# Kernel tuning notes

Hardware: AMD Instinct MI355X
Metric: run time of the kernel (lower is better)

Reference implementation:

```python
import jax, jax.numpy as jnp
import numpy as np

T, B, D, H = 1024, 128, 256, 256


def setup_inputs() -> dict:
    key = jax.random.key(0)
    ks = jax.random.split(key, 16)
    s_in = 1.0 / np.sqrt(D + H)  # torch Linear default init scale
    inp = {
        "inputs": jax.random.normal(ks[0], (T, B, D), dtype=jnp.float32),
        "Wf": jax.random.uniform(ks[1], (H, D + H), jnp.float32, -s_in, s_in),
        "bf": jax.random.uniform(ks[2], (H,), jnp.float32, -s_in, s_in),
        "Wi": jax.random.uniform(ks[3], (H, D + H), jnp.float32, -s_in, s_in),
        "bi": jax.random.uniform(ks[4], (H,), jnp.float32, -s_in, s_in),
        "Wg": jax.random.uniform(ks[5], (H, D + H), jnp.float32, -s_in, s_in),
        "bg": jax.random.uniform(ks[6], (H,), jnp.float32, -s_in, s_in),
        "Wo": jax.random.uniform(ks[7], (H, D + H), jnp.float32, -s_in, s_in),
        "bo": jax.random.uniform(ks[8], (H,), jnp.float32, -s_in, s_in),
        # estimator params stacked over the 4 gates (order: f, i, g, o)
        "estW1": jax.random.uniform(ks[9], (4, 8, H), jnp.float32, -1/np.sqrt(H), 1/np.sqrt(H)),
        "estb1": jax.random.uniform(ks[10], (4, 8), jnp.float32, -1/np.sqrt(H), 1/np.sqrt(H)),
        "estW2": jax.random.uniform(ks[11], (4, 4, 8), jnp.float32, -1/np.sqrt(8), 1/np.sqrt(8)),
        "estb2": jax.random.uniform(ks[12], (4, 4), jnp.float32, -1/np.sqrt(8), 1/np.sqrt(8)),
        "estW3": jax.random.uniform(ks[13], (4, 1, 4), jnp.float32, -0.5, 0.5),
        "estb3": jax.random.uniform(ks[14], (4, 1), jnp.float32, -0.5, 0.5),
    }
    return inp


def reference(inputs, Wf, bf, Wi, bi, Wg, bg, Wo, bo,
              estW1, estb1, estW2, estb2, estW3, estb3):
    def est(x, k):
        # tiny MLP: H -> 8 -> 4 -> 1 with tanh/tanh/sigmoid
        h1 = jnp.tanh(x @ estW1[k].T + estb1[k])
        h2 = jnp.tanh(h1 @ estW2[k].T + estb2[k])
        return jax.nn.sigmoid(h2 @ estW3[k].T + estb3[k])  # [B, 1]

    def step(carry, x):
        hx, cx = carry
        comb = jnp.concatenate([x, hx], axis=1)  # [B, D+H]
        f = jax.nn.sigmoid(comb @ Wf.T + bf)
        i = jax.nn.sigmoid(comb @ Wi.T + bi)
        g = jnp.tanh(comb @ Wg.T + bg)
        o = jax.nn.sigmoid(comb @ Wo.T + bo)
        f = f * est(f, 0)
        i = i * est(i, 1)
        g = g * est(g, 2)
        o = o * est(o, 3)
        cx = f * cx + i * g
        hx = o * jnp.tanh(cx)
        return (hx, cx), hx

    hx0 = jnp.zeros((B, H), dtype=inputs.dtype)
    cx0 = jnp.zeros((B, H), dtype=inputs.dtype)
    (hx, cx), stacked = jax.lax.scan(step, (hx0, cx0), inputs)
    return stacked, hx, cx
```

## Files before the change

### kernel.cpp

```cpp
#include <hip/hip_runtime.h>
#include <hip/hip_fp16.h>
#include <math.h>

#define T_STEPS 1024
#define BATCH   128
#define D_IN    256
#define H_DIM   256
#define NCOL    1024

typedef _Float16 half2_t __attribute__((ext_vector_type(2)));

__device__ __forceinline__ float sigmoidf_(float x) {
    return 1.0f / (1.0f + __expf(-x));
}

__device__ __forceinline__ float tanhf_(float x) {
    float ax = fabsf(x);
    float t = __expf(-2.0f * ax);
    float r = (1.0f - t) / (1.0f + t);
    return copysignf(r, x);
}

__device__ __forceinline__ float dot2f(unsigned int w, unsigned int h, float acc) {
#if __has_builtin(__builtin_amdgcn_fdot2)
    return __builtin_amdgcn_fdot2(__builtin_bit_cast(half2_t, w),
                                  __builtin_bit_cast(half2_t, h), acc, false);
#else
    __half2 wv = *(__half2*)&w, hv = *(__half2*)&h;
    acc = fmaf(__half2float(wv.x), __half2float(hv.x), acc);
    return fmaf(__half2float(wv.y), __half2float(hv.y), acc);
#endif
}

__device__ __forceinline__ unsigned int packh2(float a, float b) {
    __half2 p = __floats2half2_rn(a, b);
    return *(unsigned int*)&p;
}

__global__ __launch_bounds__(256) void prep_kernel(
    const float* __restrict__ Wf, const float* __restrict__ Wi,
    const float* __restrict__ Wg, const float* __restrict__ Wo,
    const float* __restrict__ bf, const float* __restrict__ bi,
    const float* __restrict__ bg, const float* __restrict__ bo,
    unsigned int* __restrict__ WX2, uint4* __restrict__ WX4,
    uint4* __restrict__ WH4, float* __restrict__ biasc)
{
    int idx = blockIdx.x * 256 + threadIdx.x;
    int m = idx >> 10;
    int j = idx & 1023;
    int g = j >> 8;
    int h = j & 255;
    const float* W = (g == 0) ? Wf : (g == 1) ? Wi : (g == 2) ? Wg : Wo;
    const float* row = W + h * (D_IN + H_DIM);
    const float* rx = row + 8 * m;
    const float* rh = row + D_IN + 8 * m;
    uint4 vx = make_uint4(packh2(rx[0], rx[1]), packh2(rx[2], rx[3]),
                          packh2(rx[4], rx[5]), packh2(rx[6], rx[7]));
    uint4 vh = make_uint4(packh2(rh[0], rh[1]), packh2(rh[2], rh[3]),
                          packh2(rh[4], rh[5]), packh2(rh[6], rh[7]));
    WX4[idx] = vx;
    WH4[idx] = vh;
    unsigned int* d = (unsigned int*)&vx;
    #pragma unroll
    for (int p = 0; p < 4; p++) WX2[(4 * m + p) * 1024 + j] = d[p];
    if (idx < NCOL) {
        const float* bb = (g == 0) ? bf : (g == 1) ? bi : (g == 2) ? bg : bo;
        biasc[j] = bb[h];
    }
}

__global__ __launch_bounds__(256) void pregemm_kernel(
    const float* __restrict__ x, const unsigned int* __restrict__ WX2,
    const float* __restrict__ biasc, float* __restrict__ pre) {
    __shared__ float xs[16 * 256];
    const int tid = threadIdx.x;
    const size_t r0 = (size_t)blockIdx.x * 16;

    {
        const float4* xsrc = (const float4*)(x + r0 * D_IN);
        float4* xd = (float4*)xs;
        #pragma unroll
        for (int i = 0; i < 4; i++) xd[tid + 256 * i] = xsrc[tid + 256 * i];
    }
    float4 b4 = ((const float4*)biasc)[tid];
    float a[16][4];
    #pragma unroll
    for (int r = 0; r < 16; r++) {
        a[r][0] = b4.x; a[r][1] = b4.y; a[r][2] = b4.z; a[r][3] = b4.w;
    }
    __syncthreads();

    const uint4* wp = (const uint4*)WX2;
    const float2* xs2 = (const float2*)xs;
    #pragma unroll 2
    for (int k2 = 0; k2 < 128; k2++) {
        uint4 wv = wp[k2 * 256 + tid];
        __half2 q0 = *(__half2*)&wv.x, q1 = *(__half2*)&wv.y;
        __half2 q2 = *(__half2*)&wv.z, q3 = *(__half2*)&wv.w;
        float w0l = __half2float(q0.x), w0h = __half2float(q0.y);
        float w1l = __half2float(q1.x), w1h = __half2float(q1.y);
        float w2l = __half2float(q2.x), w2h = __half2float(q2.y);
        float w3l = __half2float(q3.x), w3h = __half2float(q3.y);
        #pragma unroll
        for (int r = 0; r < 16; r++) {
            float2 xv = xs2[r * 128 + k2];
            a[r][0] = fmaf(xv.x, w0l, a[r][0]); a[r][0] = fmaf(xv.y, w0h, a[r][0]);
            a[r][1] = fmaf(xv.x, w1l, a[r][1]); a[r][1] = fmaf(xv.y, w1h, a[r][1]);
            a[r][2] = fmaf(xv.x, w2l, a[r][2]); a[r][2] = fmaf(xv.y, w2h, a[r][2]);
            a[r][3] = fmaf(xv.x, w3l, a[r][3]); a[r][3] = fmaf(xv.y, w3h, a[r][3]);
        }
    }
    #pragma unroll
    for (int r = 0; r < 16; r++) {
        ((float4*)(pre + (r0 + r) * NCOL))[tid] =
            make_float4(a[r][0], a[r][1], a[r][2], a[r][3]);
    }
}

__global__ __launch_bounds__(1024) void qlstm_kernel(
    const float* __restrict__ x,
    const uint4* __restrict__ WX4,
    const uint4* __restrict__ WH4,
    const float* __restrict__ biasc,
    const float* __restrict__ pre, int use_pre,
    const float* __restrict__ estW1, const float* __restrict__ estb1,
    const float* __restrict__ estW2, const float* __restrict__ estb2,
    const float* __restrict__ estW3, const float* __restrict__ estb3,
    float* __restrict__ out)
{
    __shared__ __align__(16) __half hxh[H_DIM];
    __shared__ __align__(16) __half hxl[H_DIM];
    __shared__ __align__(16) __half cxh[D_IN];
    __shared__ __align__(16) __half cxl[D_IN];
    __shared__ __align__(16) float gact[NCOL];
    __shared__ float w1[4][8][H_DIM];
    __shared__ float sb1[32];
    __shared__ float sW2[128];
    __shared__ float sb2[16];
    __shared__ float sW3[16];
    __shared__ float sb3[4];
    __shared__ float escale[4];

    const int b    = blockIdx.x;
    const int tid  = threadIdx.x;
    const int w    = tid >> 6;
    const int lane = tid & 63;

    for (int i = tid; i < 4 * 8 * H_DIM; i += 1024) {
        int p = i & 255;
        int base = i & ~255;
        int h = 4 * (p & 63) + (p >> 6);
        ((float*)w1)[i] = estW1[base + h];
    }
    if (tid < 32)  sb1[tid] = estb1[tid];
    if (tid < 128) sW2[tid] = estW2[tid];
    if (tid < 16)  { sb2[tid] = estb2[tid]; sW3[tid] = estW3[tid]; }
    if (tid < 4)   sb3[tid] = estb3[tid];
    if (tid < H_DIM) {
        hxh[tid] = __float2half(0.0f);
        hxl[tid] = __float2half(0.0f);
    }
    float c_reg = 0.0f, h_reg = 0.0f;
    const float b_j = use_pre ? 0.0f : biasc[tid];
    __syncthreads();

    const uint4* hh = (const uint4*)hxh;
    const uint4* hl = (const uint4*)hxl;
    const uint4* xh = (const uint4*)cxh;
    const uint4* xl = (const uint4*)cxl;

    const float* prep_ = pre + (size_t)b * NCOL + tid;
    float pnext = use_pre ? prep_[0] : 0.0f;

    for (int t = 0; t < T_STEPS; t++) {
        float aH, aL = 0.0f;
        if (use_pre) {
            aH = pnext;
            if (t + 1 < T_STEPS)
                pnext = prep_[(size_t)(t + 1) * BATCH * NCOL];
        } else {
            aH = b_j;
            if (tid < D_IN) {
                float xv = x[((size_t)t * BATCH + b) * D_IN + tid];
                __half hi = __float2half_rn(xv);
                cxh[tid] = hi;
                cxl[tid] = __float2half_rn(xv - __half2float(hi));
            }
            __syncthreads();
            #pragma unroll 4
            for (int m = 0; m < 32; m++) {
                uint4 wv = WX4[(m << 10) + tid];
                uint4 hv = xh[m], lv = xl[m];
                aH = dot2f(wv.x, hv.x, aH); aH = dot2f(wv.y, hv.y, aH);
                aH = dot2f(wv.z, hv.z, aH); aH = dot2f(wv.w, hv.w, aH);
                aL = dot2f(wv.x, lv.x, aL); aL = dot2f(wv.y, lv.y, aL);
                aL = dot2f(wv.z, lv.z, aL); aL = dot2f(wv.w, lv.w, aL);
            }
        }

        #pragma unroll 4
        for (int m = 0; m < 32; m++) {
            uint4 wv = WH4[(m << 10) + tid];
            uint4 hv = hh[m], lv = hl[m];
            aH = dot2f(wv.x, hv.x, aH); aH = dot2f(wv.y, hv.y, aH);
            aH = dot2f(wv.z, hv.z, aH); aH = dot2f(wv.w, hv.w, aH);
            aL = dot2f(wv.x, lv.x, aL); aL = dot2f(wv.y, lv.y, aL);
            aL = dot2f(wv.z, lv.z, aL); aL = dot2f(wv.w, lv.w, aL);
        }
        float acc = aH + aL;

        float v = (tid >= 512 && tid < 768) ? tanhf_(acc) : sigmoidf_(acc);
        gact[tid] = v;
        __syncthreads();

        if (tid < 256) {
            float4 gv = ((const float4*)(gact + (w << 8)))[lane];
            float h1[8];
            #pragma unroll
            for (int j = 0; j < 8; j++) {
                const float* wr = &w1[w][j][0];
                float s = fmaf(gv.x, wr[lane],
                          fmaf(gv.y, wr[lane + 64],
                          fmaf(gv.z, wr[lane + 128], gv.w * wr[lane + 192])));
                #pragma unroll
                for (int m2 = 1; m2 < 64; m2 <<= 1) s += __shfl_xor(s, m2, 64);
                h1[j] = tanhf_(s + sb1[w * 8 + j]);
            }
            float h2[4];
            #pragma unroll
            for (int j = 0; j < 4; j++) {
                float s = sb2[w * 4 + j];
                #pragma unroll
                for (int q = 0; q < 8; q++) s = fmaf(h1[q], sW2[w * 32 + j * 8 + q], s);
                h2[j] = tanhf_(s);
            }
            float s3 = sb3[w];
            #pragma unroll
            for (int q = 0; q < 4; q++) s3 = fmaf(h2[q], sW3[w * 4 + q], s3);
            if (lane == 0) escale[w] = sigmoidf_(s3);
        }
        __syncthreads();

        if (tid < 256) {
            float f  = gact[tid]       * escale[0];
            float ii = gact[256 + tid] * escale[1];
            float gg = gact[512 + tid] * escale[2];
            float o  = gact[768 + tid] * escale[3];
            c_reg = fmaf(f, c_reg, ii * gg);
            h_reg = o * tanhf_(c_reg);
            __half hi = __float2half_rn(h_reg);
            hxh[tid] = hi;
            hxl[tid] = __float2half_rn(h_reg - __half2float(hi));
            out[((size_t)t * BATCH + b) * H_DIM + tid] = h_reg;
        }
        __syncthreads();
    }

    if (tid < 256) {
        const size_t stacked = (size_t)T_STEPS * BATCH * H_DIM;
        out[stacked + (size_t)b * H_DIM + tid] = h_reg;
        out[stacked + (size_t)BATCH * H_DIM + (size_t)b * H_DIM + tid] = c_reg;
    }
}

extern "C" void kernel_launch(void* const* d_in, const int* in_sizes, int n_in,
                              void* d_out, int out_size, void* d_ws, size_t ws_size,
                              hipStream_t stream) {
    const float* x     = (const float*)d_in[0];
    const float* Wf    = (const float*)d_in[1];
    const float* bf    = (const float*)d_in[2];
    const float* Wi    = (const float*)d_in[3];
    const float* bi    = (const float*)d_in[4];
    const float* Wg    = (const float*)d_in[5];
    const float* bg    = (const float*)d_in[6];
    const float* Wo    = (const float*)d_in[7];
    const float* bo    = (const float*)d_in[8];
    const float* estW1 = (const float*)d_in[9];
    const float* estb1 = (const float*)d_in[10];
    const float* estW2 = (const float*)d_in[11];
    const float* estb2 = (const float*)d_in[12];
    const float* estW3 = (const float*)d_in[13];
    const float* estb3 = (const float*)d_in[14];

    unsigned int* WX2 = (unsigned int*)d_ws;
    uint4* WX4   = (uint4*)(WX2 + 128 * 1024);
    uint4* WH4   = WX4 + 32 * 1024;
    float* biasc = (float*)(WH4 + 32 * 1024);
    float* pre   = biasc + NCOL;

    const size_t need = (size_t)128 * 1024 * 4 * 3 + NCOL * 4 +
                        (size_t)T_STEPS * BATCH * NCOL * 4;
    const int use_pre = (ws_size >= need) ? 1 : 0;

    prep_kernel<<<128, 256, 0, stream>>>(Wf, Wi, Wg, Wo, bf, bi, bg, bo,
                                         WX2, WX4, WH4, biasc);
    if (use_pre) {
        pregemm_kernel<<<(T_STEPS * BATCH) / 16, 256, 0, stream>>>(x, WX2, biasc, pre);
    }
    qlstm_kernel<<<BATCH, 1024, 0, stream>>>(x, WX4, WH4, biasc, pre, use_pre,
                                             estW1, estb1, estW2, estb2, estW3, estb3,
                                             (float*)d_out);
}
```

Measured before the change: 10.40 ms.

## Split recurrent matvec across paired blocks with flag-based inter-block sync

Each batch row now runs on two workgroups. One computes half of the hidden-to-gate dot products and publishes the partial sums through global memory, while the other computes the other half plus the gate activations, the estimator MLP and the cell update. The two exchange partial sums and half of the hidden state through device-scope atomics and spin-wait flags. The aim is to use 256 CUs instead of 128 and halve the serial per-step matvec, at the cost of a cross-block handshake every timestep and a reliance on both blocks of a pair being co-resident. A large dummy shared array looks intended to force one block per CU.

```diff
diff --git a/kernel.cpp b/kernel.cpp
--- a/kernel.cpp
+++ b/kernel.cpp
@@ -37,15 +37,26 @@
     return *(unsigned int*)&p;
 }
 
+__device__ __forceinline__ unsigned int packhl(float v) {
+    __half hi = __float2half_rn(v);
+    __half lo = __float2half_rn(v - __half2float(hi));
+    __half2 p; p.x = hi; p.y = lo;
+    return *(unsigned int*)&p;
+}
+
 __global__ __launch_bounds__(256) void prep_kernel(
     const float* __restrict__ Wf, const float* __restrict__ Wi,
     const float* __restrict__ Wg, const float* __restrict__ Wo,
     const float* __restrict__ bf, const float* __restrict__ bi,
     const float* __restrict__ bg, const float* __restrict__ bo,
     unsigned int* __restrict__ WX2, uint4* __restrict__ WX4,
-    uint4* __restrict__ WH4, float* __restrict__ biasc)
+    uint4* __restrict__ WH4, float* __restrict__ biasc,
+    int* __restrict__ flags)
 {
     int idx = blockIdx.x * 256 + threadIdx.x;
+    if (idx < 8192) {
+        __hip_atomic_store(&flags[idx], 0, __ATOMIC_RELAXED, __HIP_MEMORY_SCOPE_AGENT);
+    }
     int m = idx >> 10;
     int j = idx & 1023;
     int g = j >> 8;
@@ -117,12 +128,189 @@
     }
 }
 
-__global__ __launch_bounds__(1024) void qlstm_kernel(
+__global__ __launch_bounds__(1024) void qlstm_pair_kernel(
+    const uint4* __restrict__ WH4,
+    const float* __restrict__ pre,
+    float* __restrict__ partial,
+    unsigned int* __restrict__ hxbuf,
+    int* __restrict__ flags,
+    const float* __restrict__ estW1, const float* __restrict__ estb1,
+    const float* __restrict__ estW2, const float* __restrict__ estb2,
+    const float* __restrict__ estW3, const float* __restrict__ estb3,
+    float* __restrict__ out)
+{
+    __shared__ __align__(16) __half hxh[128];
+    __shared__ __align__(16) __half hxl[128];
+    __shared__ __align__(16) float gact[NCOL];
+    __shared__ float w1[4][8][H_DIM];
+    __shared__ float sb1[32];
+    __shared__ float sW2[128];
+    __shared__ float sb2[16];
+    __shared__ float sW3[16];
+    __shared__ float sb3[4];
+    __shared__ float escale[4];
+    __shared__ float xpad[12288];
+
+    const int b    = blockIdx.x >> 1;
+    const int role = blockIdx.x & 1;
+    const int tid  = threadIdx.x;
+
+    if (blockIdx.x == 0x7FFFFFFF) ((volatile float*)xpad)[tid] = 1.0f;
+
+    int* flagA = flags + b * 32;
+    int* flagB = flags + 4096 + b * 32;
+    float* part_p = partial + (size_t)b * NCOL + tid;
+    unsigned int* hx_p = hxbuf + (size_t)b * 128;
+
+    if (tid < 128) { hxh[tid] = __float2half(0.0f); hxl[tid] = __float2half(0.0f); }
+
+    const uint4* hh = (const uint4*)hxh;
+    const uint4* hl = (const uint4*)hxl;
+
+    if (role == 0) {
+        __syncthreads();
+        const uint4* Wlo = WH4;
+        for (int t = 0; t < T_STEPS; t++) {
+            float aH = 0.0f, aL = 0.0f;
+            #pragma unroll
+            for (int m = 0; m < 16; m++) {
+                uint4 wv = Wlo[(m << 10) + tid];
+                uint4 hv = hh[m], lv = hl[m];
+                aH = dot2f(wv.x, hv.x, aH); aH = dot2f(wv.y, hv.y, aH);
+                aH = dot2f(wv.z, hv.z, aH); aH = dot2f(wv.w, hv.w, aH);
+                aL = dot2f(wv.x, lv.x, aL); aL = dot2f(wv.y, lv.y, aL);
+                aL = dot2f(wv.z, lv.z, aL); aL = dot2f(wv.w, lv.w, aL);
+            }
+            __hip_atomic_store(part_p, aH + aL, __ATOMIC_RELAXED, __HIP_MEMORY_SCOPE_AGENT);
+            __syncthreads();
+            if (tid == 0)
+                __hip_atomic_store(flagA, t + 1, __ATOMIC_RELEASE, __HIP_MEMORY_SCOPE_AGENT);
+            if (t + 1 < T_STEPS) {
+                if (tid == 0) {
+                    while (__hip_atomic_load(flagB, __ATOMIC_ACQUIRE,
+                                             __HIP_MEMORY_SCOPE_AGENT) < t + 1)
+                        __builtin_amdgcn_s_sleep(1);
+                }
+                __syncthreads();
+                if (tid < 128) {
+                    unsigned int u = __hip_atomic_load(&hx_p[tid], __ATOMIC_RELAXED,
+                                                       __HIP_MEMORY_SCOPE_AGENT);
+                    __half2 p = *(__half2*)&u;
+                    hxh[tid] = p.x; hxl[tid] = p.y;
+                }
+                __syncthreads();
+            }
+        }
+        return;
+    }
+
+    const int w    = tid >> 6;
+    const int lane = tid & 63;
+
+    for (int i = tid; i < 4 * 8 * H_DIM; i += 1024) {
+        int p = i & 255;
+        int base = i & ~255;
+        int h = 4 * (p & 63) + (p >> 6);
+        ((float*)w1)[i] = estW1[base + h];
+    }
+    if (tid < 32)  sb1[tid] = estb1[tid];
+    if (tid < 128) sW2[tid] = estW2[tid];
+    if (tid < 16)  { sb2[tid] = estb2[tid]; sW3[tid] = estW3[tid]; }
+    if (tid < 4)   sb3[tid] = estb3[tid];
+    float c_reg = 0.0f, h_reg = 0.0f;
+    __syncthreads();
+
+    const uint4* Whi = WH4 + (16 << 10);
+    const float* prep_ = pre + (size_t)b * NCOL + tid;
+    float pnext = prep_[0];
+
+    for (int t = 0; t < T_STEPS; t++) {
+        float aH = pnext, aL = 0.0f;
+        if (t + 1 < T_STEPS)
+            pnext = prep_[(size_t)(t + 1) * BATCH * NCOL];
+        #pragma unroll
+        for (int m = 0; m < 16; m++) {
+            uint4 wv = Whi[(m << 10) + tid];
+            uint4 hv = hh[m], lv = hl[m];
+            aH = dot2f(wv.x, hv.x, aH); aH = dot2f(wv.y, hv.y, aH);
+            aH = dot2f(wv.z, hv.z, aH); aH = dot2f(wv.w, hv.w, aH);
+            aL = dot2f(wv.x, lv.x, aL); aL = dot2f(wv.y, lv.y, aL);
+            aL = dot2f(wv.z, lv.z, aL); aL = dot2f(wv.w, lv.w, aL);
+        }
+        if (tid == 0) {
+            while (__hip_atomic_load(flagA, __ATOMIC_ACQUIRE,
+                                     __HIP_MEMORY_SCOPE_AGENT) < t + 1)
+                __builtin_amdgcn_s_sleep(1);
+        }
+        __syncthreads();
+        float pA = __hip_atomic_load(part_p, __ATOMIC_RELAXED, __HIP_MEMORY_SCOPE_AGENT);
+        float acc = aH + aL + pA;
+
+        float v = (tid >= 512 && tid < 768) ? tanhf_(acc) : sigmoidf_(acc);
+        gact[tid] = v;
+        __syncthreads();
+
+        if (tid < 256) {
+            float4 gv = ((const float4*)(gact + (w << 8)))[lane];
+            float h1[8];
+            #pragma unroll
+            for (int j = 0; j < 8; j++) {
+                const float* wr = &w1[w][j][0];
+                float s = fmaf(gv.x, wr[lane],
+                          fmaf(gv.y, wr[lane + 64],
+                          fmaf(gv.z, wr[lane + 128], gv.w * wr[lane + 192])));
+                #pragma unroll
+                for (int m2 = 1; m2 < 64; m2 <<= 1) s += __shfl_xor(s, m2, 64);
+                h1[j] = tanhf_(s + sb1[w * 8 + j]);
+            }
+            float h2[4];
+            #pragma unroll
+            for (int j = 0; j < 4; j++) {
+                float s = sb2[w * 4 + j];
+                #pragma unroll
+                for (int q = 0; q < 8; q++) s = fmaf(h1[q], sW2[w * 32 + j * 8 + q], s);
+                h2[j] = tanhf_(s);
+            }
+            float s3 = sb3[w];
+            #pragma unroll
+            for (int q = 0; q < 4; q++) s3 = fmaf(h2[q], sW3[w * 4 + q], s3);
+            if (lane == 0) escale[w] = sigmoidf_(s3);
+        }
+        __syncthreads();
+
+        if (tid < 256) {
+            float f  = gact[tid]       * escale[0];
+            float ii = gact[256 + tid] * escale[1];
+            float gg = gact[512 + tid] * escale[2];
+            float o  = gact[768 + tid] * escale[3];
+            c_reg = fmaf(f, c_reg, ii * gg);
+            h_reg = o * tanhf_(c_reg);
+            out[((size_t)t * BATCH + b) * H_DIM + tid] = h_reg;
+            unsigned int u = packhl(h_reg);
+            if (tid < 128) {
+                __hip_atomic_store(&hx_p[tid], u, __ATOMIC_RELAXED, __HIP_MEMORY_SCOPE_AGENT);
+            } else {
+                __half2 p = *(__half2*)&u;
+                hxh[tid - 128] = p.x; hxl[tid - 128] = p.y;
+            }
+        }
+        __syncthreads();
+        if (tid == 0)
+            __hip_atomic_store(flagB, t + 1, __ATOMIC_RELEASE, __HIP_MEMORY_SCOPE_AGENT);
+    }
+
+    if (tid < 256) {
+        const size_t stacked = (size_t)T_STEPS * BATCH * H_DIM;
+        out[stacked + (size_t)b * H_DIM + tid] = h_reg;
+        out[stacked + (size_t)BATCH * H_DIM + (size_t)b * H_DIM + tid] = c_reg;
+    }
+}
+
+__global__ __launch_bounds__(1024) void qlstm_fallback_kernel(
     const float* __restrict__ x,
     const uint4* __restrict__ WX4,
     const uint4* __restrict__ WH4,
     const float* __restrict__ biasc,
-    const float* __restrict__ pre, int use_pre,
     const float* __restrict__ estW1, const float* __restrict__ estb1,
     const float* __restrict__ estW2, const float* __restrict__ estb2,
     const float* __restrict__ estW3, const float* __restrict__ estb3,
@@ -161,7 +349,7 @@
         hxl[tid] = __float2half(0.0f);
     }
     float c_reg = 0.0f, h_reg = 0.0f;
-    const float b_j = use_pre ? 0.0f : biasc[tid];
+    const float b_j = biasc[tid];
     __syncthreads();
 
     const uint4* hh = (const uint4*)hxh;
@@ -169,35 +357,24 @@
     const uint4* xh = (const uint4*)cxh;
     const uint4* xl = (const uint4*)cxl;
 
-    const float* prep_ = pre + (size_t)b * NCOL + tid;
-    float pnext = use_pre ? prep_[0] : 0.0f;
-
     for (int t = 0; t < T_STEPS; t++) {
-        float aH, aL = 0.0f;
-        if (use_pre) {
-            aH = pnext;
-            if (t + 1 < T_STEPS)
-                pnext = prep_[(size_t)(t + 1) * BATCH * NCOL];
-        } else {
-            aH = b_j;
-            if (tid < D_IN) {
-                float xv = x[((size_t)t * BATCH + b) * D_IN + tid];
-                __half hi = __float2half_rn(xv);
-                cxh[tid] = hi;
-                cxl[tid] = __float2half_rn(xv - __half2float(hi));
-            }
-            __syncthreads();
-            #pragma unroll 4
-            for (int m = 0; m < 32; m++) {
-                uint4 wv = WX4[(m << 10) + tid];
-                uint4 hv = xh[m], lv = xl[m];
-                aH = dot2f(wv.x, hv.x, aH); aH = dot2f(wv.y, hv.y, aH);
-                aH = dot2f(wv.z, hv.z, aH); aH = dot2f(wv.w, hv.w, aH);
-                aL = dot2f(wv.x, lv.x, aL); aL = dot2f(wv.y, lv.y, aL);
-                aL = dot2f(wv.z, lv.z, aL); aL = dot2f(wv.w, lv.w, aL);
-            }
-        }
-
+        float aH = b_j, aL = 0.0f;
+        if (tid < D_IN) {
+            float xv = x[((size_t)t * BATCH + b) * D_IN + tid];
+            __half hi = __float2half_rn(xv);
+            cxh[tid] = hi;
+            cxl[tid] = __float2half_rn(xv - __half2float(hi));
+        }
+        __syncthreads();
+        #pragma unroll 4
+        for (int m = 0; m < 32; m++) {
+            uint4 wv = WX4[(m << 10) + tid];
+            uint4 hv = xh[m], lv = xl[m];
+            aH = dot2f(wv.x, hv.x, aH); aH = dot2f(wv.y, hv.y, aH);
+            aH = dot2f(wv.z, hv.z, aH); aH = dot2f(wv.w, hv.w, aH);
+            aL = dot2f(wv.x, lv.x, aL); aL = dot2f(wv.y, lv.y, aL);
+            aL = dot2f(wv.z, lv.z, aL); aL = dot2f(wv.w, lv.w, aL);
+        }
         #pragma unroll 4
         for (int m = 0; m < 32; m++) {
             uint4 wv = WH4[(m << 10) + tid];
@@ -283,21 +460,28 @@
     const float* estb3 = (const float*)d_in[14];
 
     unsigned int* WX2 = (unsigned int*)d_ws;
-    uint4* WX4   = (uint4*)(WX2 + 128 * 1024);
-    uint4* WH4   = WX4 + 32 * 1024;
-    float* biasc = (float*)(WH4 + 32 * 1024);
-    float* pre   = biasc + NCOL;
-
-    const size_t need = (size_t)128 * 1024 * 4 * 3 + NCOL * 4 +
-                        (size_t)T_STEPS * BATCH * NCOL * 4;
-    const int use_pre = (ws_size >= need) ? 1 : 0;
+    uint4* WX4    = (uint4*)(WX2 + 128 * 1024);
+    uint4* WH4    = WX4 + 32 * 1024;
+    float* biasc  = (float*)(WH4 + 32 * 1024);
+    int*   flags  = (int*)(biasc + NCOL);
+    float* partial= (float*)(flags + 8192);
+    unsigned int* hxbuf = (unsigned int*)(partial + (size_t)BATCH * NCOL);
+    float* pre    = (float*)(hxbuf + (size_t)BATCH * 128);
+
+    const size_t fixed = (size_t)(512 + 512 + 512 + 4 + 32 + 512 + 64) * 1024;
+    const size_t need  = fixed + (size_t)T_STEPS * BATCH * NCOL * 4;
+    const int use_pre  = (ws_size >= need) ? 1 : 0;
 
     prep_kernel<<<128, 256, 0, stream>>>(Wf, Wi, Wg, Wo, bf, bi, bg, bo,
-                                         WX2, WX4, WH4, biasc);
+                                         WX2, WX4, WH4, biasc, flags);
     if (use_pre) {
         pregemm_kernel<<<(T_STEPS * BATCH) / 16, 256, 0, stream>>>(x, WX2, biasc, pre);
-    }
-    qlstm_kernel<<<BATCH, 1024, 0, stream>>>(x, WX4, WH4, biasc, pre, use_pre,
-                                             estW1, estb1, estW2, estb2, estW3, estb3,
-                                             (float*)d_out);
-}
+        qlstm_pair_kernel<<<2 * BATCH, 1024, 0, stream>>>(
+            WH4, pre, partial, hxbuf, flags,
+            estW1, estb1, estW2, estb2, estW3, estb3, (float*)d_out);
+    } else {
+        qlstm_fallback_kernel<<<BATCH, 1024, 0, stream>>>(
+            x, WX4, WH4, biasc,
+            estW1, estb1, estW2, estb2, estW3, estb3, (float*)d_out);
+    }
+}
```

Measured after the change: 10.25 ms. About the same (-1.5%).

## Split LSTM recurrence across four cooperating blocks with register-resident weights

Applied to the files above, without the earlier changes.

Replaces the one-block-per-batch recurrence (which used a precomputed input GEMM) with groups of four 1024-thread blocks per pair of batch rows. Two blocks compute input projections into a ring buffer ahead of time, and two blocks split the hidden-state GEMV. Each block holds its quarter of the fp16 weights in registers. The blocks exchange partial sums through global memory with acquire/release flags. This removes the per-step weight reloads and the large pre-GEMM traffic, at the cost of inter-block spin synchronisation every step and a requirement that all 256 blocks be co-resident.

```diff
diff --git a/kernel.cpp b/kernel.cpp
--- a/kernel.cpp
+++ b/kernel.cpp
@@ -7,6 +7,7 @@
 #define D_IN    256
 #define H_DIM   256
 #define NCOL    1024
+#define RING    4
 
 typedef _Float16 half2_t __attribute__((ext_vector_type(2)));
 
@@ -37,92 +38,309 @@
     return *(unsigned int*)&p;
 }
 
+__device__ __forceinline__ uint4 pack8(const float* p) {
+    return make_uint4(packh2(p[0], p[1]), packh2(p[2], p[3]),
+                      packh2(p[4], p[5]), packh2(p[6], p[7]));
+}
+
+#define AQ __HIP_MEMORY_SCOPE_AGENT
+__device__ __forceinline__ void st_rel(int* p, int v) {
+    __hip_atomic_store(p, v, __ATOMIC_RELEASE, AQ);
+}
+__device__ __forceinline__ int ld_acq(int* p) {
+    return __hip_atomic_load(p, __ATOMIC_ACQUIRE, AQ);
+}
+__device__ __forceinline__ void stf(float* p, float v) {
+    __hip_atomic_store(p, v, __ATOMIC_RELAXED, AQ);
+}
+__device__ __forceinline__ float ldf(const float* p) {
+    return __hip_atomic_load((float*)p, __ATOMIC_RELAXED, AQ);
+}
+
+__device__ __forceinline__ void gemv_q(const uint4* wreg, const uint4* SH,
+                                       const uint4* SL, float bias,
+                                       float& p0, float& p1) {
+    float a0H = bias, a0L = 0.0f, a1H = bias, a1L = 0.0f;
+    #pragma unroll
+    for (int m = 0; m < 16; m++) {
+        uint4 wv = wreg[m];
+        uint4 h0 = SH[m],      l0 = SL[m];
+        uint4 h1 = SH[16 + m], l1 = SL[16 + m];
+        a0H = dot2f(wv.x, h0.x, a0H); a0H = dot2f(wv.y, h0.y, a0H);
+        a0H = dot2f(wv.z, h0.z, a0H); a0H = dot2f(wv.w, h0.w, a0H);
+        a0L = dot2f(wv.x, l0.x, a0L); a0L = dot2f(wv.y, l0.y, a0L);
+        a0L = dot2f(wv.z, l0.z, a0L); a0L = dot2f(wv.w, l0.w, a0L);
+        a1H = dot2f(wv.x, h1.x, a1H); a1H = dot2f(wv.y, h1.y, a1H);
+        a1H = dot2f(wv.z, h1.z, a1H); a1H = dot2f(wv.w, h1.w, a1H);
+        a1L = dot2f(wv.x, l1.x, a1L); a1L = dot2f(wv.y, l1.y, a1L);
+        a1L = dot2f(wv.z, l1.z, a1L); a1L = dot2f(wv.w, l1.w, a1L);
+    }
+    p0 = a0H + a0L;
+    p1 = a1H + a1L;
+}
+
 __global__ __launch_bounds__(256) void prep_kernel(
     const float* __restrict__ Wf, const float* __restrict__ Wi,
     const float* __restrict__ Wg, const float* __restrict__ Wo,
     const float* __restrict__ bf, const float* __restrict__ bi,
     const float* __restrict__ bg, const float* __restrict__ bo,
-    unsigned int* __restrict__ WX2, uint4* __restrict__ WX4,
-    uint4* __restrict__ WH4, float* __restrict__ biasc)
+    int quad_mode,
+    uint4* __restrict__ WQ4, uint4* __restrict__ WX4,
+    uint4* __restrict__ WH4, float* __restrict__ biasc,
+    int* __restrict__ flags)
 {
     int idx = blockIdx.x * 256 + threadIdx.x;
-    int m = idx >> 10;
-    int j = idx & 1023;
-    int g = j >> 8;
-    int h = j & 255;
-    const float* W = (g == 0) ? Wf : (g == 1) ? Wi : (g == 2) ? Wg : Wo;
-    const float* row = W + h * (D_IN + H_DIM);
-    const float* rx = row + 8 * m;
-    const float* rh = row + D_IN + 8 * m;
-    uint4 vx = make_uint4(packh2(rx[0], rx[1]), packh2(rx[2], rx[3]),
-                          packh2(rx[4], rx[5]), packh2(rx[6], rx[7]));
-    uint4 vh = make_uint4(packh2(rh[0], rh[1]), packh2(rh[2], rh[3]),
-                          packh2(rh[4], rh[5]), packh2(rh[6], rh[7]));
-    WX4[idx] = vx;
-    WH4[idx] = vh;
-    unsigned int* d = (unsigned int*)&vx;
-    #pragma unroll
-    for (int p = 0; p < 4; p++) WX2[(4 * m + p) * 1024 + j] = d[p];
-    if (idx < NCOL) {
+    if (quad_mode && idx < 16384) {
+        __hip_atomic_store(&flags[idx], 0, __ATOMIC_RELAXED, AQ);
+    }
+    if (idx < 1024) {
+        int g = idx >> 8, h = idx & 255;
         const float* bb = (g == 0) ? bf : (g == 1) ? bi : (g == 2) ? bg : bo;
-        biasc[j] = bb[h];
-    }
-}
-
-__global__ __launch_bounds__(256) void pregemm_kernel(
-    const float* __restrict__ x, const unsigned int* __restrict__ WX2,
-    const float* __restrict__ biasc, float* __restrict__ pre) {
-    __shared__ float xs[16 * 256];
+        biasc[idx] = bb[h];
+    }
+    if (quad_mode) {
+        if (idx < 65536) {
+            int q = idx >> 14, m = (idx >> 10) & 15, j = idx & 1023;
+            int g = j >> 8, h = j & 255;
+            const float* W = (g == 0) ? Wf : (g == 1) ? Wi : (g == 2) ? Wg : Wo;
+            const float* row = W + h * (D_IN + H_DIM);
+            int base = ((q < 2) ? q * 128 : 256 + (q - 2) * 128) + 8 * m;
+            WQ4[idx] = pack8(row + base);
+        } else {
+            int e = idx - 65536;
+            int which = e >> 15;
+            int e2 = e & 32767;
+            int m = e2 >> 10, j = e2 & 1023;
+            int g = j >> 8, h = j & 255;
+            const float* W = (g == 0) ? Wf : (g == 1) ? Wi : (g == 2) ? Wg : Wo;
+            const float* row = W + h * (D_IN + H_DIM);
+            if (which == 0) WX4[e2] = pack8(row + 8 * m);
+            else            WH4[e2] = pack8(row + D_IN + 8 * m);
+        }
+    } else {
+        if (idx < 32768) {
+            int m = idx >> 10, j = idx & 1023;
+            int g = j >> 8, h = j & 255;
+            const float* W = (g == 0) ? Wf : (g == 1) ? Wi : (g == 2) ? Wg : Wo;
+            WX4[idx] = pack8(W + h * (D_IN + H_DIM) + 8 * m);
+        } else if (idx < 65536) {
+            int e2 = idx - 32768;
+            int m = e2 >> 10, j = e2 & 1023;
+            int g = j >> 8, h = j & 255;
+            const float* W = (g == 0) ? Wf : (g == 1) ? Wi : (g == 2) ? Wg : Wo;
+            WH4[e2] = pack8(W + h * (D_IN + H_DIM) + D_IN + 8 * m);
+        }
+    }
+}
+
+__global__ __launch_bounds__(1024, 1) void qlstm_quad_kernel(
+    const float* __restrict__ x,
+    const uint4* __restrict__ WQ4,
+    const float* __restrict__ biasc,
+    float* __restrict__ hpart,
+    float* __restrict__ xring,
+    int* __restrict__ flags,
+    const float* __restrict__ estW1, const float* __restrict__ estb1,
+    const float* __restrict__ estW2, const float* __restrict__ estb2,
+    const float* __restrict__ estW3, const float* __restrict__ estb3,
+    float* __restrict__ out)
+{
+    __shared__ __align__(16) float gact[2 * NCOL];
+    __shared__ float w1p[4 * 8 * H_DIM];
+    __shared__ float sb1[32];
+    __shared__ float sW2[128];
+    __shared__ float sb2[16];
+    __shared__ float sW3[16];
+    __shared__ float sb3[4];
+    __shared__ float escl[8];
+    __shared__ __align__(16) __half slh[2 * 128];
+    __shared__ __align__(16) __half sll[2 * 128];
+
+    const int Q   = blockIdx.x >> 2;
+    const int q   = blockIdx.x & 3;
     const int tid = threadIdx.x;
-    const size_t r0 = (size_t)blockIdx.x * 16;
-
+
+    uint4 wreg[16];
     {
-        const float4* xsrc = (const float4*)(x + r0 * D_IN);
-        float4* xd = (float4*)xs;
+        const uint4* wp = WQ4 + ((size_t)q << 14) + tid;
         #pragma unroll
-        for (int i = 0; i < 4; i++) xd[tid + 256 * i] = xsrc[tid + 256 * i];
-    }
-    float4 b4 = ((const float4*)biasc)[tid];
-    float a[16][4];
-    #pragma unroll
-    for (int r = 0; r < 16; r++) {
-        a[r][0] = b4.x; a[r][1] = b4.y; a[r][2] = b4.z; a[r][3] = b4.w;
-    }
+        for (int m = 0; m < 16; m++) wreg[m] = wp[(size_t)m << 10];
+    }
+
+    const uint4* SH = (const uint4*)slh;
+    const uint4* SL = (const uint4*)sll;
+
+    if (q < 2) {
+        const int d0 = q * 128;
+        float* myring = xring + (size_t)(Q * 2 + q) * (RING * 2048);
+        int* myflag = &flags[Q * 32 + q];
+        int* cfA = &flags[8192 + Q * 32 + 0];
+        int* cfB = &flags[8192 + Q * 32 + 1];
+        const float bload = (q == 0) ? biasc[tid] : 0.0f;
+
+        float xv_nxt = 0.0f;
+        if (tid < 256) {
+            int r = tid >> 7, kk = tid & 127;
+            xv_nxt = x[(size_t)(2 * Q + r) * D_IN + d0 + kk];
+        }
+        for (int t = 0; t < T_STEPS; t++) {
+            if (tid == 0) {
+                for (;;) {
+                    int ca = ld_acq(cfA), cb = ld_acq(cfB);
+                    int cm = ca < cb ? ca : cb;
+                    if (t - cm < RING) break;
+                    __builtin_amdgcn_s_sleep(8);
+                }
+            }
+            __syncthreads();
+            float xv = xv_nxt;
+            if (tid < 256) {
+                int r = tid >> 7, kk = tid & 127;
+                __half hi = __float2half_rn(xv);
+                slh[(r << 7) + kk] = hi;
+                sll[(r << 7) + kk] = __float2half_rn(xv - __half2float(hi));
+                if (t + 1 < T_STEPS)
+                    xv_nxt = x[((size_t)(t + 1) * BATCH + (2 * Q + r)) * D_IN + d0 + kk];
+            }
+            __syncthreads();
+            float p0, p1;
+            gemv_q(wreg, SH, SL, bload, p0, p1);
+            float* dst = myring + (t & (RING - 1)) * 2048;
+            stf(&dst[tid], p0);
+            stf(&dst[1024 + tid], p1);
+            __syncthreads();
+            if (tid == 0) st_rel(myflag, t + 1);
+        }
+        return;
+    }
+
+    const int cu = q - 2;
+    const int kq = cu << 7;
+    float* myhp_b   = hpart + (size_t)(Q * 2 + cu) * 4096;
+    float* peerhp_b = hpart + (size_t)(Q * 2 + (1 - cu)) * 4096;
+    int* myhf   = &flags[4096 + Q * 32 + cu];
+    int* peerhf = &flags[4096 + Q * 32 + (1 - cu)];
+    int* mycf   = &flags[8192 + Q * 32 + cu];
+    int* xf0 = &flags[Q * 32 + 0];
+    int* xf1 = &flags[Q * 32 + 1];
+    const float* ring0 = xring + (size_t)(Q * 2 + 0) * (RING * 2048);
+    const float* ring1 = xring + (size_t)(Q * 2 + 1) * (RING * 2048);
+
+    for (int i = tid; i < 4 * 8 * H_DIM; i += 1024) {
+        int p = i & 255;
+        int base = i & ~255;
+        int h = 4 * (p & 63) + (p >> 6);
+        w1p[i] = estW1[base + h];
+    }
+    if (tid < 32)  sb1[tid] = estb1[tid];
+    if (tid < 128) sW2[tid] = estW2[tid];
+    if (tid < 16)  { sb2[tid] = estb2[tid]; sW3[tid] = estW3[tid]; }
+    if (tid < 4)   sb3[tid] = estb3[tid];
+    if (tid < 256) { slh[tid] = __float2half(0.0f); sll[tid] = __float2half(0.0f); }
+    float c_reg = 0.0f, h_reg = 0.0f;
     __syncthreads();
 
-    const uint4* wp = (const uint4*)WX2;
-    const float2* xs2 = (const float2*)xs;
-    #pragma unroll 2
-    for (int k2 = 0; k2 < 128; k2++) {
-        uint4 wv = wp[k2 * 256 + tid];
-        __half2 q0 = *(__half2*)&wv.x, q1 = *(__half2*)&wv.y;
-        __half2 q2 = *(__half2*)&wv.z, q3 = *(__half2*)&wv.w;
-        float w0l = __half2float(q0.x), w0h = __half2float(q0.y);
-        float w1l = __half2float(q1.x), w1h = __half2float(q1.y);
-        float w2l = __half2float(q2.x), w2h = __half2float(q2.y);
-        float w3l = __half2float(q3.x), w3h = __half2float(q3.y);
-        #pragma unroll
-        for (int r = 0; r < 16; r++) {
-            float2 xv = xs2[r * 128 + k2];
-            a[r][0] = fmaf(xv.x, w0l, a[r][0]); a[r][0] = fmaf(xv.y, w0h, a[r][0]);
-            a[r][1] = fmaf(xv.x, w1l, a[r][1]); a[r][1] = fmaf(xv.y, w1h, a[r][1]);
-            a[r][2] = fmaf(xv.x, w2l, a[r][2]); a[r][2] = fmaf(xv.y, w2h, a[r][2]);
-            a[r][3] = fmaf(xv.x, w3l, a[r][3]); a[r][3] = fmaf(xv.y, w3h, a[r][3]);
-        }
-    }
-    #pragma unroll
-    for (int r = 0; r < 16; r++) {
-        ((float4*)(pre + (r0 + r) * NCOL))[tid] =
-            make_float4(a[r][0], a[r][1], a[r][2], a[r][3]);
-    }
-}
-
-__global__ __launch_bounds__(1024) void qlstm_kernel(
+    for (int t = 0; t < T_STEPS; t++) {
+        float p0, p1;
+        gemv_q(wreg, SH, SL, 0.0f, p0, p1);
+        const int par = t & 1;
+        float* myhp = myhp_b + par * 2048;
+        stf(&myhp[tid], p0);
+        stf(&myhp[1024 + tid], p1);
+        __syncthreads();
+        if (tid == 0) st_rel(myhf, t + 1);
+        if (tid == 0) {
+            while (ld_acq(peerhf) < t + 1) __builtin_amdgcn_s_sleep(1);
+        } else if (tid == 64) {
+            while (ld_acq(xf0) < t + 1) __builtin_amdgcn_s_sleep(1);
+        } else if (tid == 128) {
+            while (ld_acq(xf1) < t + 1) __builtin_amdgcn_s_sleep(1);
+        }
+        __syncthreads();
+        const int slot = t & (RING - 1);
+        const float* r0p = ring0 + slot * 2048;
+        const float* r1p = ring1 + slot * 2048;
+        const float* pr  = peerhp_b + par * 2048;
+        float xa0 = ldf(&r0p[tid]),        xb0 = ldf(&r1p[tid]);
+        float xa1 = ldf(&r0p[1024 + tid]), xb1 = ldf(&r1p[1024 + tid]);
+        float ph0 = ldf(&pr[tid]),         ph1 = ldf(&pr[1024 + tid]);
+        float hA0 = (cu == 0) ? p0 : ph0,  hB0 = (cu == 0) ? ph0 : p0;
+        float hA1 = (cu == 0) ? p1 : ph1,  hB1 = (cu == 0) ? ph1 : p1;
+        float tot0 = ((xa0 + xb0) + hA0) + hB0;
+        float tot1 = ((xa1 + xb1) + hA1) + hB1;
+        const int gate = tid >> 8;
+        gact[tid]        = (gate == 2) ? tanhf_(tot0) : sigmoidf_(tot0);
+        gact[1024 + tid] = (gate == 2) ? tanhf_(tot1) : sigmoidf_(tot1);
+        __syncthreads();
+
+        if (tid < 512) {
+            const int w_   = tid >> 6;
+            const int row  = w_ >> 2, ge = w_ & 3;
+            const int lane = tid & 63;
+            float4 gv = ((const float4*)(gact + row * 1024 + (ge << 8)))[lane];
+            float h1[8];
+            #pragma unroll
+            for (int j = 0; j < 8; j++) {
+                const float* wr = &w1p[(ge * 8 + j) * H_DIM];
+                float s = fmaf(gv.x, wr[lane],
+                          fmaf(gv.y, wr[lane + 64],
+                          fmaf(gv.z, wr[lane + 128], gv.w * wr[lane + 192])));
+                #pragma unroll
+                for (int m2 = 1; m2 < 64; m2 <<= 1) s += __shfl_xor(s, m2, 64);
+                h1[j] = tanhf_(s + sb1[ge * 8 + j]);
+            }
+            float h2[4];
+            #pragma unroll
+            for (int j = 0; j < 4; j++) {
+                float s = sb2[ge * 4 + j];
+                #pragma unroll
+                for (int p = 0; p < 8; p++) s = fmaf(h1[p], sW2[ge * 32 + j * 8 + p], s);
+                h2[j] = tanhf_(s);
+            }
+            float s3 = sb3[ge];
+            #pragma unroll
+            for (int p = 0; p < 4; p++) s3 = fmaf(h2[p], sW3[ge * 4 + p], s3);
+            if (lane == 0) escl[row * 4 + ge] = sigmoidf_(s3);
+        }
+        __syncthreads();
+
+        if (tid < 512) {
+            const int r = tid >> 8, j = tid & 255;
+            const float* ga = gact + r * 1024;
+            const float* es = escl + r * 4;
+            float f  = ga[j]       * es[0];
+            float ii = ga[256 + j] * es[1];
+            float gg = ga[512 + j] * es[2];
+            float o  = ga[768 + j] * es[3];
+            c_reg = fmaf(f, c_reg, ii * gg);
+            h_reg = o * tanhf_(c_reg);
+            if (r == cu)
+                out[((size_t)t * BATCH + (2 * Q + r)) * H_DIM + j] = h_reg;
+            if (j >= kq && j < kq + 128) {
+                __half hi = __float2half_rn(h_reg);
+                slh[(r << 7) + (j - kq)] = hi;
+                sll[(r << 7) + (j - kq)] = __float2half_rn(h_reg - __half2float(hi));
+            }
+        }
+        __syncthreads();
+        if (tid == 0) st_rel(mycf, t + 1);
+    }
+
+    if (tid < 512) {
+        const int r = tid >> 8, j = tid & 255;
+        if (r == cu) {
+            const size_t stacked = (size_t)T_STEPS * BATCH * H_DIM;
+            out[stacked + (size_t)(2 * Q + r) * H_DIM + j] = h_reg;
+            out[stacked + (size_t)BATCH * H_DIM + (size_t)(2 * Q + r) * H_DIM + j] = c_reg;
+        }
+    }
+}
+
+__global__ __launch_bounds__(1024) void qlstm_fallback_kernel(
     const float* __restrict__ x,
     const uint4* __restrict__ WX4,
     const uint4* __restrict__ WH4,
     const float* __restrict__ biasc,
-    const float* __restrict__ pre, int use_pre,
     const float* __restrict__ estW1, const float* __restrict__ estb1,
     const float* __restrict__ estW2, const float* __restrict__ estb2,
     const float* __restrict__ estW3, const float* __restrict__ estb3,
@@ -161,7 +379,7 @@
         hxl[tid] = __float2half(0.0f);
     }
     float c_reg = 0.0f, h_reg = 0.0f;
-    const float b_j = use_pre ? 0.0f : biasc[tid];
+    const float b_j = biasc[tid];
     __syncthreads();
 
     const uint4* hh = (const uint4*)hxh;
@@ -169,35 +387,24 @@
     const uint4* xh = (const uint4*)cxh;
     const uint4* xl = (const uint4*)cxl;
 
-    const float* prep_ = pre + (size_t)b * NCOL + tid;
-    float pnext = use_pre ? prep_[0] : 0.0f;
-
     for (int t = 0; t < T_STEPS; t++) {
-        float aH, aL = 0.0f;
-        if (use_pre) {
-            aH = pnext;
-            if (t + 1 < T_STEPS)
-                pnext = prep_[(size_t)(t + 1) * BATCH * NCOL];
-        } else {
-            aH = b_j;
-            if (tid < D_IN) {
-                float xv = x[((size_t)t * BATCH + b) * D_IN + tid];
-                __half hi = __float2half_rn(xv);
-                cxh[tid] = hi;
-                cxl[tid] = __float2half_rn(xv - __half2float(hi));
-            }
-            __syncthreads();
-            #pragma unroll 4
-            for (int m = 0; m < 32; m++) {
-                uint4 wv = WX4[(m << 10) + tid];
-                uint4 hv = xh[m], lv = xl[m];
-                aH = dot2f(wv.x, hv.x, aH); aH = dot2f(wv.y, hv.y, aH);
-                aH = dot2f(wv.z, hv.z, aH); aH = dot2f(wv.w, hv.w, aH);
-                aL = dot2f(wv.x, lv.x, aL); aL = dot2f(wv.y, lv.y, aL);
-                aL = dot2f(wv.z, lv.z, aL); aL = dot2f(wv.w, lv.w, aL);
-            }
-        }
-
+        float aH = b_j, aL = 0.0f;
+        if (tid < D_IN) {
+            float xv = x[((size_t)t * BATCH + b) * D_IN + tid];
+            __half hi = __float2half_rn(xv);
+            cxh[tid] = hi;
+            cxl[tid] = __float2half_rn(xv - __half2float(hi));
+        }
+        __syncthreads();
+        #pragma unroll 4
+        for (int m = 0; m < 32; m++) {
+            uint4 wv = WX4[(m << 10) + tid];
+            uint4 hv = xh[m], lv = xl[m];
+            aH = dot2f(wv.x, hv.x, aH); aH = dot2f(wv.y, hv.y, aH);
+            aH = dot2f(wv.z, hv.z, aH); aH = dot2f(wv.w, hv.w, aH);
+            aL = dot2f(wv.x, lv.x, aL); aL = dot2f(wv.y, lv.y, aL);
+            aL = dot2f(wv.z, lv.z, aL); aL = dot2f(wv.w, lv.w, aL);
+        }
         #pragma unroll 4
         for (int m = 0; m < 32; m++) {
             uint4 wv = WH4[(m << 10) + tid];
@@ -231,12 +438,12 @@
             for (int j = 0; j < 4; j++) {
                 float s = sb2[w * 4 + j];
                 #pragma unroll
-                for (int q = 0; q < 8; q++) s = fmaf(h1[q], sW2[w * 32 + j * 8 + q], s);
+                for (int p = 0; p < 8; p++) s = fmaf(h1[p], sW2[w * 32 + j * 8 + p], s);
                 h2[j] = tanhf_(s);
             }
             float s3 = sb3[w];
             #pragma unroll
-            for (int q = 0; q < 4; q++) s3 = fmaf(h2[q], sW3[w * 4 + q], s3);
+            for (int p = 0; p < 4; p++) s3 = fmaf(h2[p], sW3[w * 4 + p], s3);
             if (lane == 0) escale[w] = sigmoidf_(s3);
         }
         __syncthreads();
@@ -282,22 +489,30 @@
     const float* estW3 = (const float*)d_in[13];
     const float* estb3 = (const float*)d_in[14];
 
-    unsigned int* WX2 = (unsigned int*)d_ws;
-    uint4* WX4   = (uint4*)(WX2 + 128 * 1024);
-    uint4* WH4   = WX4 + 32 * 1024;
-    float* biasc = (float*)(WH4 + 32 * 1024);
-    float* pre   = biasc + NCOL;
-
-    const size_t need = (size_t)128 * 1024 * 4 * 3 + NCOL * 4 +
-                        (size_t)T_STEPS * BATCH * NCOL * 4;
-    const int use_pre = (ws_size >= need) ? 1 : 0;
-
-    prep_kernel<<<128, 256, 0, stream>>>(Wf, Wi, Wg, Wo, bf, bi, bg, bo,
-                                         WX2, WX4, WH4, biasc);
-    if (use_pre) {
-        pregemm_kernel<<<(T_STEPS * BATCH) / 16, 256, 0, stream>>>(x, WX2, biasc, pre);
-    }
-    qlstm_kernel<<<BATCH, 1024, 0, stream>>>(x, WX4, WH4, biasc, pre, use_pre,
-                                             estW1, estb1, estW2, estb2, estW3, estb3,
-                                             (float*)d_out);
-}
+    uint4* WQ4    = (uint4*)d_ws;
+    uint4* WX4q   = WQ4 + 65536;
+    uint4* WH4q   = WX4q + 32768;
+    float* biascq = (float*)(WH4q + 32768);
+    int*   flags  = (int*)(biascq + 1024);
+    float* hpart  = (float*)(flags + 16384);
+    float* xring  = hpart + (size_t)64 * 8192;
+    const size_t need_quad = (size_t)131072 * 16 + 1024 * 4 + 16384 * 4 +
+                             (size_t)64 * 8192 * 4 + (size_t)64 * 2 * RING * 2048 * 4;
+
+    if (ws_size >= need_quad) {
+        prep_kernel<<<512, 256, 0, stream>>>(Wf, Wi, Wg, Wo, bf, bi, bg, bo,
+                                             1, WQ4, WX4q, WH4q, biascq, flags);
+        qlstm_quad_kernel<<<256, 1024, 0, stream>>>(
+            x, WQ4, biascq, hpart, xring, flags,
+            estW1, estb1, estW2, estb2, estW3, estb3, (float*)d_out);
+    } else {
+        uint4* WX4f   = (uint4*)d_ws;
+        uint4* WH4f   = WX4f + 32768;
+        float* biascf = (float*)(WH4f + 32768);
+        prep_kernel<<<512, 256, 0, stream>>>(Wf, Wi, Wg, Wo, bf, bi, bg, bo,
+                                             0, WX4f, WX4f, WH4f, biascf, (int*)biascf);
+        qlstm_fallback_kernel<<<BATCH, 1024, 0, stream>>>(
+            x, WX4f, WH4f, biascf,
+            estW1, estb1, estW2, estb2, estW3, estb3, (float*)d_out);
+    }
+}
```

Measured after the change: 20.21 ms. +94.3%, slower.
